# Performance work log

Hardware: AMD Instinct MI355X
Metric: run time of the kernel (lower is better)

The kernel has to match this reference:

```python
import jax, jax.numpy as jnp
import numpy as np

EMBD_DIM = 1024
NUM_HEADS = 16
HEAD_DIM = EMBD_DIM // NUM_HEADS


def setup_inputs() -> dict:
    key = jax.random.key(0)
    ks = jax.random.split(key, 9)
    B, S, D = 2, 2048, EMBD_DIM
    scale = 1.0 / np.sqrt(D)
    return {
        "x": jax.random.normal(ks[0], (B, S, D), dtype=jnp.float32),
        "wq": jax.random.normal(ks[1], (D, D), dtype=jnp.float32) * scale,
        "bq": jnp.zeros((D,), dtype=jnp.float32),
        "wk": jax.random.normal(ks[2], (D, D), dtype=jnp.float32) * scale,
        "bk": jnp.zeros((D,), dtype=jnp.float32),
        "wv": jax.random.normal(ks[3], (D, D), dtype=jnp.float32) * scale,
        "bv": jnp.zeros((D,), dtype=jnp.float32),
        "wo": jax.random.normal(ks[4], (D, D), dtype=jnp.float32) * scale,
        "bo": jnp.zeros((D,), dtype=jnp.float32),
    }


def reference(x, wq, bq, wk, bk, wv, bv, wo, bo):
    B, S, D = x.shape
    H, hd = NUM_HEADS, HEAD_DIM
    # projections: weights stored as (in, out) so y = x @ w + b
    q = (x @ wq + bq).reshape(B, S, H, hd).transpose(0, 2, 1, 3)  # [B,H,S,hd]
    k = (x @ wk + bk).reshape(B, S, H, hd).transpose(0, 2, 1, 3)
    v = (x @ wv + bv).reshape(B, S, H, hd).transpose(0, 2, 1, 3)
    scores = jnp.einsum("bhqd,bhkd->bhqk", q, k) / jnp.sqrt(jnp.float32(hd))
    causal = jnp.tril(jnp.ones((S, S), dtype=bool))  # [S,S]
    neg = jnp.finfo(scores.dtype).min
    scores = jnp.where(causal[None, None, :, :], scores, neg)
    attn = jax.nn.softmax(scores, axis=-1)
    out = jnp.einsum("bhqk,bhkd->bhqd", attn, v)  # [B,H,S,hd]
    out = out.transpose(0, 2, 1, 3).reshape(B, S, D)
    return out @ wo + bo
```

## Files before the change

### kernel.cpp

```cpp
#include <hip/hip_runtime.h>
#include <math.h>

#define S_LEN 2048
#define BATCH 2
#define DMODEL 1024
#define NHEADS 16
#define MROWS 4096

typedef short bf8 __attribute__((ext_vector_type(8)));
typedef short bf4 __attribute__((ext_vector_type(4)));
typedef float f32x4 __attribute__((ext_vector_type(4)));
typedef unsigned short u16;

static __device__ inline u16 f2bf(float f) {
    union { float f; unsigned u; } v; v.f = f;
    unsigned r = v.u + 0x7fffu + ((v.u >> 16) & 1u);
    return (u16)(r >> 16);
}

static __device__ inline void load16(const void* g, void* l) {
    __builtin_amdgcn_global_load_lds(
        (const __attribute__((address_space(1))) unsigned int*)g,
        (__attribute__((address_space(3))) unsigned int*)l, 16, 0, 0);
}

__global__ __launch_bounds__(256) void prep_kernel(
    const float* __restrict__ x, u16* __restrict__ xb,
    const float* __restrict__ W0, const float* __restrict__ W1,
    const float* __restrict__ W2, const float* __restrict__ W3,
    u16* __restrict__ wT) {
    const int bx = blockIdx.x, t = threadIdx.x;
    if (bx < 2048) {
        int i = bx * 256 + t;
        const float4* p = (const float4*)x + (size_t)i * 2;
        float4 a = p[0], b = p[1];
        u16 tmp[8] = {f2bf(a.x), f2bf(a.y), f2bf(a.z), f2bf(a.w),
                      f2bf(b.x), f2bf(b.y), f2bf(b.z), f2bf(b.w)};
        ((uint4*)xb)[i] = *(uint4*)tmp;
        return;
    }
    __shared__ u16 Ls[64][65];
    const int id = bx - 2048;
    const int z = id >> 8, rem = id & 255;
    const int n0 = (rem & 15) * 64, k0 = (rem >> 4) * 64;
    const float* W = z == 0 ? W0 : z == 1 ? W1 : z == 2 ? W2 : W3;
    u16* Wt = wT + (size_t)z * 1024 * 1024;
    const int r = t >> 2, c4 = (t & 3) * 16;
    const float* p = W + (size_t)(k0 + r) * 1024 + n0 + c4;
#pragma unroll
    for (int i = 0; i < 16; i += 4) {
        float4 v = *(const float4*)(p + i);
        Ls[r][c4 + i + 0] = f2bf(v.x);
        Ls[r][c4 + i + 1] = f2bf(v.y);
        Ls[r][c4 + i + 2] = f2bf(v.z);
        Ls[r][c4 + i + 3] = f2bf(v.w);
    }
    __syncthreads();
    u16 tmp[16];
#pragma unroll
    for (int i = 0; i < 16; i++) tmp[i] = Ls[c4 + i][r];
    uint4* q = (uint4*)(Wt + (size_t)(n0 + r) * 1024 + k0 + c4);
    q[0] = *(uint4*)tmp;
    q[1] = *(uint4*)(tmp + 8);
}

template <int MODE>
__global__ __launch_bounds__(256) void gemm_mfma(
    const u16* __restrict__ A, const u16* __restrict__ Bt,
    const float* __restrict__ bqp, const float* __restrict__ bkp,
    const float* __restrict__ bvp,
    u16* __restrict__ qout, u16* __restrict__ kout, u16* __restrict__ vtout,
    float* __restrict__ fout, float qscale) {
    __shared__ __align__(16) u16 As[128 * 64];
    __shared__ __align__(16) u16 Bs[128 * 64];

    const int t = threadIdx.x, lane = t & 63, w = t >> 6;
    const int quad = lane >> 4, l16 = lane & 15;
    const int wr = w >> 1, wc = w & 1;
    const int row0 = blockIdx.y * 128, col0 = blockIdx.x * 128;
    const int K = DMODEL;

    const int srow = t >> 3;
    const int ksw = ((t & 7) ^ (srow & 7)) * 8;
    const u16* ag = A + (size_t)(row0 + srow) * K + ksw;
    const u16* bg = Bt + (size_t)(col0 + srow) * K + ksw;
    const int swz = l16 & 7;

    f32x4 acc[4][4] = {};

    u16* lA = As + (size_t)(w * 8) * 64;
    u16* lB = Bs + (size_t)(w * 8) * 64;

    for (int it = 0; it < 16; ++it) {
        if (it) __syncthreads();
        const int k0 = it * 64;
#pragma unroll
        for (int i = 0; i < 4; i++) {
            load16(ag + (size_t)i * 32 * K + k0, lA + i * 32 * 64);
            load16(bg + (size_t)i * 32 * K + k0, lB + i * 32 * 64);
        }
        __syncthreads();
#pragma unroll
        for (int kc = 0; kc < 2; kc++) {
            bf8 xf[4], wf[4];
#pragma unroll
            for (int ni = 0; ni < 4; ni++)
                xf[ni] = *(const bf8*)&As[(wr * 64 + ni * 16 + l16) * 64 +
                                          ((kc * 4 + quad) ^ swz) * 8];
#pragma unroll
            for (int mi = 0; mi < 4; mi++)
                wf[mi] = *(const bf8*)&Bs[(wc * 64 + mi * 16 + l16) * 64 +
                                          ((kc * 4 + quad) ^ swz) * 8];
#pragma unroll
            for (int mi = 0; mi < 4; mi++)
#pragma unroll
                for (int ni = 0; ni < 4; ni++)
                    acc[mi][ni] = __builtin_amdgcn_mfma_f32_16x16x32_bf16(
                        wf[mi], xf[ni], acc[mi][ni], 0, 0, 0);
        }
    }

    const int sect = (col0 + wc * 64) >> 10;
#pragma unroll
    for (int mi = 0; mi < 4; mi++) {
        const int featb = col0 + wc * 64 + mi * 16 + quad * 4;
        float b4[4];
#pragma unroll
        for (int reg = 0; reg < 4; reg++)
            b4[reg] = (MODE == 1 ? bqp : (sect == 0 ? bqp : sect == 1 ? bkp : bvp))
                          [(featb + reg) & 1023];
#pragma unroll
        for (int ni = 0; ni < 4; ni++) {
            const int xrow = row0 + wr * 64 + ni * 16 + l16;
            if (MODE == 1) {
                float4 o;
                o.x = acc[mi][ni][0] + b4[0];
                o.y = acc[mi][ni][1] + b4[1];
                o.z = acc[mi][ni][2] + b4[2];
                o.w = acc[mi][ni][3] + b4[3];
                *(float4*)(fout + (size_t)xrow * 1024 + featb) = o;
            } else {
                const int cf = featb & 1023;
                if (sect == 0) {
                    u16 t4[4];
#pragma unroll
                    for (int reg = 0; reg < 4; reg++)
                        t4[reg] = f2bf((acc[mi][ni][reg] + b4[reg]) * qscale);
                    *(uint2*)(qout + (size_t)xrow * 1024 + cf) = *(uint2*)t4;
                } else if (sect == 1) {
                    u16 t4[4];
#pragma unroll
                    for (int reg = 0; reg < 4; reg++)
                        t4[reg] = f2bf(acc[mi][ni][reg] + b4[reg]);
                    *(uint2*)(kout + (size_t)xrow * 1024 + cf) = *(uint2*)t4;
                } else {
#pragma unroll
                    for (int reg = 0; reg < 4; reg++)
                        vtout[((size_t)(xrow >> 11) * 1024 + cf + reg) * S_LEN +
                              (xrow & 2047)] = f2bf(acc[mi][ni][reg] + b4[reg]);
                }
            }
        }
    }
}

__global__ __launch_bounds__(512, 4) void attn_kernel(
    const u16* __restrict__ Qg, const u16* __restrict__ Kg,
    const u16* __restrict__ Vt, u16* __restrict__ Og) {
    __shared__ __align__(16) u16 LdsF[2 * 16384];

    const int t = threadIdx.x, lane = t & 63, w = t >> 6;
    const int quad = lane >> 4, l16 = lane & 15;
    const int wtile = w >> 2, wq = w & 3;
    const int pi = 15 - blockIdx.y;
    const int bh = blockIdx.x, b = bh >> 4, h = bh & 15;
    const size_t base = (size_t)b * S_LEN * DMODEL + h * 64;
    const size_t vbase = ((size_t)b * 1024 + h * 64) * S_LEN;
    const int swz = (l16 >> 1) & 3;

    const int rK = lane >> 2, cc = lane & 3;
    const int ssS = (rK >> 1) & 3;
    const int chnk = (cc ^ ssS) * 8;
    const u16* src;
    size_t jstr, tstr;
    if (w < 4) {
        src = Kg + base + (size_t)((w & 1) * 64 + rK) * DMODEL +
              (w >> 1) * 32 + chnk;
        jstr = (size_t)16 * DMODEL;
        tstr = (size_t)128 * DMODEL;
    } else {
        const int wv = w - 4;
        src = Vt + vbase + (size_t)rK * S_LEN +
              (wv >> 1) * 64 + (wv & 1) * 32 + chnk;
        jstr = (size_t)16 * S_LEN;
        tstr = (size_t)128;
    }
    const int dstoff = (w * 4) * 512;

#define STAGE(bufsel, tile)                                                    \
    {                                                                          \
        u16* _d = LdsF + (bufsel) * 16384 + dstoff;                            \
        const u16* _s = src + (size_t)(tile) * tstr;                           \
        load16(_s, _d);                                                        \
        load16(_s + jstr, _d + 512);                                           \
        load16(_s + 2 * jstr, _d + 1024);                                      \
        load16(_s + 3 * jstr, _d + 1536);                                      \
    }

    const int niter = pi + 1;
    const int q0 = pi * 128 + wtile * 64;

    bf8 aq[2];
#pragma unroll
    for (int c = 0; c < 2; c++)
        aq[c] = *(const bf8*)(Qg + base +
            (size_t)(q0 + wq * 16 + l16) * DMODEL + c * 32 + quad * 8);

    float lsum = 0.f;
    f32x4 oT[4] = {};

    const int qloc = wtile * 64 + wq * 16 + l16;
    const int qmax = wtile * 64 + wq * 16 + 15;

    STAGE(0, 0)
    __syncthreads();

    for (int kt = 0; kt < niter; kt++) {
        const int cur = kt & 1;
        if (kt + 1 < niter) STAGE(cur ^ 1, kt + 1)
        const u16* KB = LdsF + cur * 16384;
        const u16* VB = KB + 8192;

        f32x4 scv[8] = {};
        __builtin_amdgcn_s_setprio(1);
#pragma unroll
        for (int c = 0; c < 2; c++)
#pragma unroll
            for (int ns = 0; ns < 8; ns++) {
                bf8 ak = *(const bf8*)&KB[(c * 128 + ns * 16 + l16) * 32 +
                                          ((quad ^ swz) * 8)];
                scv[ns] = __builtin_amdgcn_mfma_f32_16x16x32_bf16(
                    ak, aq[c], scv[ns], 0, 0, 0);
            }
        __builtin_amdgcn_s_setprio(0);

        const bool diag = (kt == niter - 1);
#pragma unroll
        for (int ns = 0; ns < 8; ns++) {
            if (diag && ns * 16 > qmax) continue;
            float p[4];
#pragma unroll
            for (int r = 0; r < 4; r++) {
                int key = ns * 16 + quad * 4 + r;
                p[r] = (diag && key > qloc) ? 0.f
                                            : __builtin_amdgcn_exp2f(scv[ns][r]);
                lsum += p[r];
            }
            union { unsigned u[2]; bf4 v; } pk;
            pk.u[0] = (__float_as_uint(p[0]) >> 16) |
                      (__float_as_uint(p[1]) & 0xffff0000u);
            pk.u[1] = (__float_as_uint(p[2]) >> 16) |
                      (__float_as_uint(p[3]) & 0xffff0000u);
            __builtin_amdgcn_s_setprio(1);
#pragma unroll
            for (int ds = 0; ds < 4; ds++) {
                bf4 av = *(const bf4*)&VB[((ns >> 1) * 64 + ds * 16 + l16) * 32 +
                    ((((ns & 1) * 2 + (quad >> 1)) ^ swz) * 8) + (quad & 1) * 4];
                oT[ds] = __builtin_amdgcn_mfma_f32_16x16x16bf16_1k(
                    av, pk.v, oT[ds], 0, 0, 0);
            }
            __builtin_amdgcn_s_setprio(0);
        }
        __syncthreads();
    }
#undef STAGE

    float l = lsum;
    l += __shfl_xor(l, 16, 64);
    l += __shfl_xor(l, 32, 64);
    const float inv = 1.f / l;
    const int qq = q0 + wq * 16 + l16;
#pragma unroll
    for (int ds = 0; ds < 4; ds++) {
        u16 t4[4];
#pragma unroll
        for (int r = 0; r < 4; r++) t4[r] = f2bf(oT[ds][r] * inv);
        *(uint2*)(Og + base + (size_t)qq * DMODEL + ds * 16 + quad * 4) =
            *(uint2*)t4;
    }
}

extern "C" void kernel_launch(void* const* d_in, const int* in_sizes, int n_in,
                              void* d_out, int out_size, void* d_ws, size_t ws_size,
                              hipStream_t stream) {
    const float* x  = (const float*)d_in[0];
    const float* wq = (const float*)d_in[1];
    const float* bq = (const float*)d_in[2];
    const float* wk = (const float*)d_in[3];
    const float* bk = (const float*)d_in[4];
    const float* wv = (const float*)d_in[5];
    const float* bv = (const float*)d_in[6];
    const float* wo = (const float*)d_in[7];
    const float* bo = (const float*)d_in[8];
    float* out = (float*)d_out;

    const size_t E = (size_t)MROWS * DMODEL;
    u16* xb  = (u16*)d_out;
    u16* vt  = xb + E;
    u16* wT  = (u16*)d_ws;
    u16* woT = wT + 3145728;
    u16* qb  = wT + 4194304;
    u16* kb  = qb + E;
    u16* ob  = kb + E;

    dim3 blk(256);
    prep_kernel<<<3072, blk, 0, stream>>>(x, xb, wq, wk, wv, wo, wT);

    gemm_mfma<0><<<dim3(24, 32), blk, 0, stream>>>(
        xb, wT, bq, bk, bv, qb, kb, vt, nullptr, 0.18033688011112042f);

    attn_kernel<<<dim3(BATCH * NHEADS, 16), dim3(512), 0, stream>>>(
        qb, kb, vt, ob);

    gemm_mfma<1><<<dim3(8, 32), blk, 0, stream>>>(
        ob, woT, bo, nullptr, nullptr, nullptr, nullptr, nullptr, out, 1.0f);
}
```

Measured before the change: 182.5 us.

## Double-buffer LDS tiles in projection GEMM to overlap loads with MFMA

```diff
diff --git a/kernel.cpp b/kernel.cpp
--- a/kernel.cpp
+++ b/kernel.cpp
@@ -71,8 +71,8 @@
     const float* __restrict__ bvp,
     u16* __restrict__ qout, u16* __restrict__ kout, u16* __restrict__ vtout,
     float* __restrict__ fout, float qscale) {
-    __shared__ __align__(16) u16 As[128 * 64];
-    __shared__ __align__(16) u16 Bs[128 * 64];
+    __shared__ __align__(16) u16 As[2][128 * 64];
+    __shared__ __align__(16) u16 Bs[2][128 * 64];
 
     const int t = threadIdx.x, lane = t & 63, w = t >> 6;
     const int quad = lane >> 4, l16 = lane & 15;
@@ -88,29 +88,37 @@
 
     f32x4 acc[4][4] = {};
 
-    u16* lA = As + (size_t)(w * 8) * 64;
-    u16* lB = Bs + (size_t)(w * 8) * 64;
-
+    const int dst = (w * 8) * 64;
+
+#define GSTAGE(bufsel, k0v)                                                    \
+    {                                                                          \
+        u16* _lA = As[bufsel] + dst;                                           \
+        u16* _lB = Bs[bufsel] + dst;                                           \
+        _Pragma("unroll")                                                      \
+        for (int i = 0; i < 4; i++) {                                          \
+            load16(ag + (size_t)i * 32 * K + (k0v), _lA + i * 32 * 64);        \
+            load16(bg + (size_t)i * 32 * K + (k0v), _lB + i * 32 * 64);        \
+        }                                                                      \
+    }
+
+    GSTAGE(0, 0)
+    __syncthreads();
+
+#pragma unroll 2
     for (int it = 0; it < 16; ++it) {
-        if (it) __syncthreads();
-        const int k0 = it * 64;
-#pragma unroll
-        for (int i = 0; i < 4; i++) {
-            load16(ag + (size_t)i * 32 * K + k0, lA + i * 32 * 64);
-            load16(bg + (size_t)i * 32 * K + k0, lB + i * 32 * 64);
-        }
-        __syncthreads();
+        const int buf = it & 1;
+        if (it + 1 < 16) GSTAGE(buf ^ 1, (it + 1) * 64)
 #pragma unroll
         for (int kc = 0; kc < 2; kc++) {
             bf8 xf[4], wf[4];
 #pragma unroll
             for (int ni = 0; ni < 4; ni++)
-                xf[ni] = *(const bf8*)&As[(wr * 64 + ni * 16 + l16) * 64 +
-                                          ((kc * 4 + quad) ^ swz) * 8];
+                xf[ni] = *(const bf8*)&As[buf][(wr * 64 + ni * 16 + l16) * 64 +
+                                              ((kc * 4 + quad) ^ swz) * 8];
 #pragma unroll
             for (int mi = 0; mi < 4; mi++)
-                wf[mi] = *(const bf8*)&Bs[(wc * 64 + mi * 16 + l16) * 64 +
-                                          ((kc * 4 + quad) ^ swz) * 8];
+                wf[mi] = *(const bf8*)&Bs[buf][(wc * 64 + mi * 16 + l16) * 64 +
+                                              ((kc * 4 + quad) ^ swz) * 8];
 #pragma unroll
             for (int mi = 0; mi < 4; mi++)
 #pragma unroll
@@ -118,7 +126,9 @@
                     acc[mi][ni] = __builtin_amdgcn_mfma_f32_16x16x32_bf16(
                         wf[mi], xf[ni], acc[mi][ni], 0, 0, 0);
         }
-    }
+        __syncthreads();
+    }
+#undef GSTAGE
 
     const int sect = (col0 + wc * 64) >> 10;
 #pragma unroll
```

Result: slower. 198.2 us (+8.6%).
